# Optimization experiments

Hardware: AMD Instinct MI355X
Metric: run time of the kernel (lower is better)

Reference implementation:

```python
import jax, jax.numpy as jnp
import numpy as np

B, N, E = 2, 50000, 800000
IN, HID, OUT = 128, 64, 1
EPS = 1e-5


def setup_inputs() -> dict:
    key = jax.random.key(0)
    ks = jax.random.split(key, 13)
    x = jax.random.normal(ks[0], (B, N, IN), jnp.float32)
    edge_index = jax.random.randint(ks[1], (2, E), 0, N, dtype=jnp.int64)
    edge_weight = 0.1 * jax.random.normal(ks[2], (E,), jnp.float32)  # nn.Parameter, pre-exp
    W1 = jax.random.normal(ks[3], (IN, HID), jnp.float32) / np.sqrt(IN)
    b1 = jnp.zeros((HID,), jnp.float32)
    W2 = jax.random.normal(ks[4], (HID, HID), jnp.float32) / np.sqrt(HID)
    b2 = jnp.zeros((HID,), jnp.float32)
    g1 = jnp.ones((HID,), jnp.float32)
    be1 = jnp.zeros((HID,), jnp.float32)
    g2 = jnp.ones((HID,), jnp.float32)
    be2 = jnp.zeros((HID,), jnp.float32)
    Wc = jax.random.normal(ks[5], (HID, OUT), jnp.float32) / np.sqrt(HID)
    bc = jnp.zeros((OUT,), jnp.float32)
    return {"x": x, "edge_weight": edge_weight, "W1": W1, "b1": b1,
            "W2": W2, "b2": b2, "g1": g1, "be1": be1, "g2": g2, "be2": be2,
            "Wc": Wc, "bc": bc, "edge_index": edge_index}


def reference(x, edge_weight, W1, b1, W2, b2, g1, be1, g2, be2, Wc, bc, edge_index):
    n = x.shape[1]
    row, col = edge_index[0], edge_index[1]
    ew = jnp.exp(edge_weight)
    # GCN normalization with self-loops (fill_value=1), as in PyG gcn_norm
    loop = jnp.arange(n)
    rows = jnp.concatenate([row, loop])
    cols = jnp.concatenate([col, loop])
    w = jnp.concatenate([ew, jnp.ones((n,), ew.dtype)])
    deg = jax.ops.segment_sum(w, cols, num_segments=n)
    dinv = 1.0 / jnp.sqrt(deg)  # deg >= 1 due to self-loops
    norm = dinv[rows] * w * dinv[cols]  # [E+N]

    def conv(h, W, b):
        h = h @ W                                  # [B, N, H]
        msg = h[:, rows, :] * norm[None, :, None]  # gather + weight  [B, E+N, H]
        agg = jnp.zeros_like(h).at[:, cols, :].add(msg)  # scatter-add
        return agg + b

    def bn(h, g, be):  # BatchNorm1d over flattened (B*N, H), training-mode stats
        h2 = h.reshape(-1, h.shape[-1])
        m = h2.mean(axis=0)
        v = h2.var(axis=0)
        return (((h2 - m) / jnp.sqrt(v + EPS)) * g + be).reshape(h.shape)

    h = jax.nn.relu(conv(x, W1, b1))
    h = bn(h, g1, be1)  # dropout is identity in eval
    h = jax.nn.relu(conv(h, W2, b2))
    h = bn(h, g2, be2)
    out = (h @ Wc + bc)[..., 0]  # squeeze(-1) -> [B, N]
    return out
```

## Files before the change

### kernel.cpp

```cpp
#include <hip/hip_runtime.h>
#include <hip/hip_fp16.h>
#include <cstdint>
#include <cstddef>


#define CAP  64
#define OCAP 65536
#define BN_EPS 1e-5f

static __device__ __forceinline__ unsigned h2u(__half2 h) {
  union { __half2 h; unsigned u; } c; c.h = h; return c.u;
}
static __device__ __forceinline__ __half2 u2h(unsigned u) {
  union { unsigned u; __half2 h; } c; c.u = u; return c.h;
}
static __device__ __forceinline__ unsigned pack_pair(int src, float w) {
  __half hw = __float2half_rn(w);
  union { __half h; unsigned short s; } c; c.h = hw;
  return ((unsigned)src << 16) | c.s;
}
static __device__ __forceinline__ float pair_w(unsigned p) {
  union { unsigned short s; __half h; } c; c.s = (unsigned short)(p & 0xFFFFu);
  return __half2float(c.h);
}

__global__ void k_mega(const float* __restrict__ x, const float* __restrict__ W,
                       __half* __restrict__ out, int nrows, int N,
                       const float* __restrict__ ew, const int* __restrict__ ei,
                       int* __restrict__ cnt, unsigned* __restrict__ pairs,
                       int* __restrict__ ofl_cnt, int* __restrict__ ofl_list,
                       int E, int gemmBlocks, int fillBlocks) {
  constexpr int RT = 64, KC = 64, S = KC + 4;
  __shared__ float ws[KC * 64];
  __shared__ float xs[RT * S];

  int bid = blockIdx.x;
  int tid = threadIdx.x;
  int role = bid % 3;

  if (role == 0) {
    int gid = bid / 3;
    if (gid >= gemmBlocks) return;
    int row0 = gid * RT;
    int rg = tid >> 4, cg = tid & 15;
    int c0 = cg * 4, r0 = rg * 4;
    float acc[4][4];
#pragma unroll
    for (int i = 0; i < 4; ++i)
#pragma unroll
      for (int j = 0; j < 4; ++j) acc[i][j] = 0.0f;

    for (int ch = 0; ch < 2; ++ch) {
      if (ch) __syncthreads();
      const float4* Wp = (const float4*)(W + (size_t)ch * KC * 64);
      for (int s = tid; s < KC * 16; s += 256)
        ((float4*)ws)[s] = Wp[s];
      for (int s = tid; s < RT * 16; s += 256) {
        int r = s >> 4, k4 = s & 15;
        int gr = row0 + r;
        float4 v = make_float4(0.f, 0.f, 0.f, 0.f);
        if (gr < nrows)
          v = *(const float4*)(x + (size_t)gr * 128 + ch * KC + k4 * 4);
        *(float4*)&xs[r * S + k4 * 4] = v;
      }
      __syncthreads();
#pragma unroll 2
      for (int kk = 0; kk < KC; kk += 4) {
        float4 wv0 = *(const float4*)&ws[(kk + 0) * 64 + c0];
        float4 wv1 = *(const float4*)&ws[(kk + 1) * 64 + c0];
        float4 wv2 = *(const float4*)&ws[(kk + 2) * 64 + c0];
        float4 wv3 = *(const float4*)&ws[(kk + 3) * 64 + c0];
#pragma unroll
        for (int i = 0; i < 4; ++i) {
          float4 xv = *(const float4*)&xs[(r0 + i) * S + kk];
          acc[i][0] = fmaf(xv.x, wv0.x, acc[i][0]);
          acc[i][1] = fmaf(xv.x, wv0.y, acc[i][1]);
          acc[i][2] = fmaf(xv.x, wv0.z, acc[i][2]);
          acc[i][3] = fmaf(xv.x, wv0.w, acc[i][3]);
          acc[i][0] = fmaf(xv.y, wv1.x, acc[i][0]);
          acc[i][1] = fmaf(xv.y, wv1.y, acc[i][1]);
          acc[i][2] = fmaf(xv.y, wv1.z, acc[i][2]);
          acc[i][3] = fmaf(xv.y, wv1.w, acc[i][3]);
          acc[i][0] = fmaf(xv.z, wv2.x, acc[i][0]);
          acc[i][1] = fmaf(xv.z, wv2.y, acc[i][1]);
          acc[i][2] = fmaf(xv.z, wv2.z, acc[i][2]);
          acc[i][3] = fmaf(xv.z, wv2.w, acc[i][3]);
          acc[i][0] = fmaf(xv.w, wv3.x, acc[i][0]);
          acc[i][1] = fmaf(xv.w, wv3.y, acc[i][1]);
          acc[i][2] = fmaf(xv.w, wv3.z, acc[i][2]);
          acc[i][3] = fmaf(xv.w, wv3.w, acc[i][3]);
        }
      }
    }
#pragma unroll
    for (int i = 0; i < 4; ++i) {
      int gr = row0 + r0 + i;
      if (gr < nrows) {
        int orow = (gr < N) ? gr * 2 : (gr - N) * 2 + 1;
        __half2 h01 = __floats2half2_rn(acc[i][0], acc[i][1]);
        __half2 h23 = __floats2half2_rn(acc[i][2], acc[i][3]);
        *(uint2*)(out + (size_t)orow * 64 + c0) = make_uint2(h2u(h01), h2u(h23));
      }
    }
  } else {
    int fid = (bid / 3) * 2 + role - 1;
    if (fid >= fillBlocks) return;
    int e = fid * 256 + tid;
    if (e >= E) return;
    int r = ei[e];
    int c = ei[(size_t)E + e];
    float w = expf(ew[e]);
    int pos = atomicAdd(&cnt[c], 1);
    if (pos < CAP) {
      pairs[(size_t)c * CAP + pos] = pack_pair(r, w);
    } else {
      int o = atomicAdd(ofl_cnt, 1);
      if (o < OCAP) ofl_list[o] = e;
    }
  }
}

__global__ void k_degb(const unsigned* __restrict__ pairs, const int* __restrict__ cnt,
                       float* __restrict__ deg, int N) {
  int node = blockIdx.x * 4 + (threadIdx.x >> 6);
  if (node >= N) return;
  int lane = threadIdx.x & 63;
  int n = cnt[node];
  n = n > CAP ? CAP : n;
  float v = 0.0f;
  if (lane < n) v = pair_w(pairs[(size_t)node * CAP + lane]);
#pragma unroll
  for (int off = 32; off > 0; off >>= 1) v += __shfl_xor(v, off, 64);
  if (lane == 0) deg[node] = v + 1.0f;
}

__global__ void k_dego(const float* __restrict__ ew, const int* __restrict__ ei,
                       const int* __restrict__ ofl_cnt, const int* __restrict__ ofl_list,
                       float* __restrict__ deg, int E) {
  int tot = *ofl_cnt;
  if (tot > OCAP) tot = OCAP;
  for (int i = blockIdx.x * blockDim.x + threadIdx.x; i < tot;
       i += gridDim.x * blockDim.x) {
    int e = ofl_list[i];
    atomicAdd(&deg[ei[(size_t)E + e]], expf(ew[e]));
  }
}

__global__ void k_dinvf(float* __restrict__ deg, int N) {
  int i = blockIdx.x * blockDim.x + threadIdx.x;
  if (i < N) deg[i] = rsqrtf(deg[i]);
}

__global__ void k_gemm2(const __half* __restrict__ in, const float* __restrict__ W,
                        __half* __restrict__ out, int nrows,
                        const float* __restrict__ bias, const float* __restrict__ scsh) {
  constexpr int RT = 64, KC = 64, S = KC + 4;
  __shared__ float ws[KC * 64];
  __shared__ float xs[RT * S];

  int tid = threadIdx.x;
  int row0 = blockIdx.x * RT;
  for (int s = tid; s < KC * 16; s += 256)
    ((float4*)ws)[s] = ((const float4*)W)[s];
  for (int s = tid; s < RT * 16; s += 256) {
    int r = s >> 4, k4 = s & 15;
    int gr = row0 + r;
    int kg = k4 * 4;
    float4 v = make_float4(0.f, 0.f, 0.f, 0.f);
    if (gr < nrows) {
      uint2 u = *(const uint2*)(in + (size_t)gr * 64 + kg);
      float2 fa = __half22float2(u2h(u.x));
      float2 fb = __half22float2(u2h(u.y));
      v = make_float4(fa.x, fa.y, fb.x, fb.y);
    }
    float4 bb = *(const float4*)(bias + kg);
    float4 sc = *(const float4*)(scsh + kg);
    float4 sh = *(const float4*)(scsh + 64 + kg);
    v.x = fmaxf(v.x + bb.x, 0.f) * sc.x + sh.x;
    v.y = fmaxf(v.y + bb.y, 0.f) * sc.y + sh.y;
    v.z = fmaxf(v.z + bb.z, 0.f) * sc.z + sh.z;
    v.w = fmaxf(v.w + bb.w, 0.f) * sc.w + sh.w;
    *(float4*)&xs[r * S + kg] = v;
  }
  __syncthreads();

  int rg = tid >> 4, cg = tid & 15;
  int c0 = cg * 4, r0 = rg * 4;
  float acc[4][4];
#pragma unroll
  for (int i = 0; i < 4; ++i)
#pragma unroll
    for (int j = 0; j < 4; ++j) acc[i][j] = 0.0f;
#pragma unroll 2
  for (int kk = 0; kk < KC; kk += 4) {
    float4 wv0 = *(const float4*)&ws[(kk + 0) * 64 + c0];
    float4 wv1 = *(const float4*)&ws[(kk + 1) * 64 + c0];
    float4 wv2 = *(const float4*)&ws[(kk + 2) * 64 + c0];
    float4 wv3 = *(const float4*)&ws[(kk + 3) * 64 + c0];
#pragma unroll
    for (int i = 0; i < 4; ++i) {
      float4 xv = *(const float4*)&xs[(r0 + i) * S + kk];
      acc[i][0] = fmaf(xv.x, wv0.x, acc[i][0]);
      acc[i][1] = fmaf(xv.x, wv0.y, acc[i][1]);
      acc[i][2] = fmaf(xv.x, wv0.z, acc[i][2]);
      acc[i][3] = fmaf(xv.x, wv0.w, acc[i][3]);
      acc[i][0] = fmaf(xv.y, wv1.x, acc[i][0]);
      acc[i][1] = fmaf(xv.y, wv1.y, acc[i][1]);
      acc[i][2] = fmaf(xv.y, wv1.z, acc[i][2]);
      acc[i][3] = fmaf(xv.y, wv1.w, acc[i][3]);
      acc[i][0] = fmaf(xv.z, wv2.x, acc[i][0]);
      acc[i][1] = fmaf(xv.z, wv2.y, acc[i][1]);
      acc[i][2] = fmaf(xv.z, wv2.z, acc[i][2]);
      acc[i][3] = fmaf(xv.z, wv2.w, acc[i][3]);
      acc[i][0] = fmaf(xv.w, wv3.x, acc[i][0]);
      acc[i][1] = fmaf(xv.w, wv3.y, acc[i][1]);
      acc[i][2] = fmaf(xv.w, wv3.z, acc[i][2]);
      acc[i][3] = fmaf(xv.w, wv3.w, acc[i][3]);
    }
  }
#pragma unroll
  for (int i = 0; i < 4; ++i) {
    int gr = row0 + r0 + i;
    if (gr < nrows) {
      __half2 h01 = __floats2half2_rn(acc[i][0], acc[i][1]);
      __half2 h23 = __floats2half2_rn(acc[i][2], acc[i][3]);
      *(uint2*)(out + (size_t)gr * 64 + c0) = make_uint2(h2u(h01), h2u(h23));
    }
  }
}

__global__ void k_agg(const __half* __restrict__ h, const unsigned* __restrict__ pairs,
                      const int* __restrict__ cnt, const float* __restrict__ dinv,
                      __half* __restrict__ raw, int N) {
  int node = blockIdx.x * 4 + (threadIdx.x >> 6);
  if (node >= N) return;
  int lane = threadIdx.x & 63;
  const __half2* hv = (const __half2*)h;
  float dc = dinv[node];
  float2 self = __half22float2(hv[(size_t)node * 64 + lane]);
  float2 acc = make_float2(self.x * dc, self.y * dc);
  int n = cnt[node];
  n = n > CAP ? CAP : n;
  const unsigned* pp = pairs + (size_t)node * CAP;
  int k = 0;
  for (; k + 12 <= n; k += 12) {
    unsigned p[12];
#pragma unroll
    for (int q = 0; q < 12; ++q) p[q] = pp[k + q];
    float dr[12];
#pragma unroll
    for (int q = 0; q < 12; ++q) dr[q] = dinv[p[q] >> 16];
    __half2 v[12];
#pragma unroll
    for (int q = 0; q < 12; ++q) v[q] = hv[(size_t)(p[q] >> 16) * 64 + lane];
#pragma unroll
    for (int q = 0; q < 12; ++q) {
      float w = pair_w(p[q]) * dr[q];
      float2 f = __half22float2(v[q]);
      acc.x = fmaf(w, f.x, acc.x);
      acc.y = fmaf(w, f.y, acc.y);
    }
  }
  for (; k + 4 <= n; k += 4) {
    unsigned p[4];
#pragma unroll
    for (int q = 0; q < 4; ++q) p[q] = pp[k + q];
    float dr[4];
#pragma unroll
    for (int q = 0; q < 4; ++q) dr[q] = dinv[p[q] >> 16];
    __half2 v[4];
#pragma unroll
    for (int q = 0; q < 4; ++q) v[q] = hv[(size_t)(p[q] >> 16) * 64 + lane];
#pragma unroll
    for (int q = 0; q < 4; ++q) {
      float w = pair_w(p[q]) * dr[q];
      float2 f = __half22float2(v[q]);
      acc.x = fmaf(w, f.x, acc.x);
      acc.y = fmaf(w, f.y, acc.y);
    }
  }
  for (; k < n; ++k) {
    unsigned p = pp[k];
    float w = pair_w(p) * dinv[p >> 16];
    float2 f = __half22float2(hv[(size_t)(p >> 16) * 64 + lane]);
    acc.x = fmaf(w, f.x, acc.x);
    acc.y = fmaf(w, f.y, acc.y);
  }
  ((__half2*)raw)[(size_t)node * 64 + lane] =
      __floats2half2_rn(acc.x * dc, acc.y * dc);
}

__global__ void k_ofl(const float* __restrict__ ew, const int* __restrict__ ei,
                      const float* __restrict__ dinv, const int* __restrict__ ofl_cnt,
                      const int* __restrict__ ofl_list,
                      const __half* __restrict__ h, __half* __restrict__ raw,
                      int N, int E) {
  int tot = *ofl_cnt;
  if (tot > OCAP) tot = OCAP;
  for (int i = blockIdx.x * blockDim.x + threadIdx.x; i < tot;
       i += gridDim.x * blockDim.x) {
    int e = ofl_list[i];
    int r = ei[e];
    int c = ei[(size_t)E + e];
    float nrm = dinv[r] * expf(ew[e]) * dinv[c];
    const __half2* hr = (const __half2*)(h + (size_t)r * 128);
    unsigned* dst = (unsigned*)(raw + (size_t)c * 128);
    for (int j = 0; j < 64; ++j) {
      float2 hv2 = __half22float2(hr[j]);
      unsigned old = dst[j], assumed;
      do {
        assumed = old;
        float2 cur = __half22float2(u2h(assumed));
        __half2 nv = __floats2half2_rn(cur.x + nrm * hv2.x, cur.y + nrm * hv2.y);
        old = atomicCAS(&dst[j], assumed, h2u(nv));
      } while (old != assumed);
    }
  }
}

__global__ void k_stats(const __half* __restrict__ raw, const float* __restrict__ bias,
                        float* __restrict__ stats, const float* __restrict__ g,
                        const float* __restrict__ be, float* __restrict__ scsh,
                        int* __restrict__ done, float invCnt, int rows) {
  __shared__ float S[256], Q[256];
  __shared__ int isLast;
  int tid = threadIdx.x;
  int c = tid & 63, rg = tid >> 6;
  float s = 0.0f, q = 0.0f;
  for (int r = blockIdx.x * 4 + rg; r < rows; r += gridDim.x * 4) {
    float y = fmaxf(__half2float(raw[(size_t)r * 64 + c]) + bias[c], 0.0f);
    s += y;
    q += y * y;
  }
  S[tid] = s; Q[tid] = q;
  __syncthreads();
  if (tid < 64) {
    float ts = S[tid] + S[tid + 64] + S[tid + 128] + S[tid + 192];
    float tq = Q[tid] + Q[tid + 64] + Q[tid + 128] + Q[tid + 192];
    atomicAdd(&stats[tid], ts);
    atomicAdd(&stats[64 + tid], tq);
  }
  __threadfence();
  if (tid == 0) {
    int old = atomicAdd(done, 1);
    isLast = (old == (int)gridDim.x - 1);
  }
  __syncthreads();
  if (isLast && tid < 64) {
    __threadfence();
    float m = atomicAdd(&stats[tid], 0.0f) * invCnt;
    float qq = atomicAdd(&stats[64 + tid], 0.0f) * invCnt;
    float v = qq - m * m;
    v = v < 0.0f ? 0.0f : v;
    float inv = rsqrtf(v + BN_EPS);
    float sc = g[tid] * inv;
    scsh[tid] = sc;
    scsh[64 + tid] = be[tid] - m * sc;
  }
}

__global__ void k_out(const __half* __restrict__ raw, const float* __restrict__ bias,
                      const float* __restrict__ scsh, const float* __restrict__ Wc,
                      const float* __restrict__ bc, float* __restrict__ out,
                      int rows, int N) {
  int row = blockIdx.x * 4 + (threadIdx.x >> 6);
  int c = threadIdx.x & 63;
  if (row >= rows) return;
  float v = fmaxf(__half2float(raw[(size_t)row * 64 + c]) + bias[c], 0.0f)
              * scsh[c] + scsh[64 + c];
  float p = v * Wc[c];
#pragma unroll
  for (int off = 32; off > 0; off >>= 1) p += __shfl_xor(p, off, 64);
  if (c == 0) {
    int node = row >> 1, b = row & 1;
    out[(size_t)b * N + node] = p + bc[0];
  }
}

extern "C" void kernel_launch(void* const* d_in, const int* in_sizes, int n_in,
                              void* d_out, int out_size, void* d_ws, size_t ws_size,
                              hipStream_t stream) {
  const float* x   = (const float*)d_in[0];
  const float* ew  = (const float*)d_in[1];
  const float* W1  = (const float*)d_in[2];
  const float* b1  = (const float*)d_in[3];
  const float* W2  = (const float*)d_in[4];
  const float* b2  = (const float*)d_in[5];
  const float* g1  = (const float*)d_in[6];
  const float* be1 = (const float*)d_in[7];
  const float* g2  = (const float*)d_in[8];
  const float* be2 = (const float*)d_in[9];
  const float* Wc  = (const float*)d_in[10];
  const float* bc  = (const float*)d_in[11];
  const int*   ei  = (const int*)d_in[12];

  const int E  = in_sizes[1];
  const int BN = in_sizes[0] / 128;
  const int N  = BN / 2;

  char* w = (char*)d_ws;
  size_t off = 0;
  int*   cnt    = (int*)  (w + off); off += (size_t)N * 4;
  float* stats1 = (float*)(w + off); off += 512;
  float* stats2 = (float*)(w + off); off += 512;
  int*   oflc   = (int*)  (w + off); off += 16;
  int*   done1  = (int*)  (w + off); off += 16;
  int*   done2  = (int*)  (w + off); off += 16;
  size_t zbytes = off;
  float* dinv   = (float*)(w + off); off += (size_t)N * 4;
  float* scsh1  = (float*)(w + off); off += 512;
  float* scsh2  = (float*)(w + off); off += 512;
  int*   ofll   = (int*)  (w + off); off += (size_t)OCAP * 4;
  off = (off + 255) & ~(size_t)255;
  unsigned* pairs = (unsigned*)(w + off); off += (size_t)N * CAP * 4;
  __half* bufA  = (__half*)(w + off); off += (size_t)BN * 64 * 2;
  __half* bufB  = (__half*)(w + off); off += (size_t)BN * 64 * 2;

  float* out = (float*)d_out;

  hipMemsetAsync(w, 0, zbytes, stream);

  dim3 blk(256);
  int gB = (BN + 63) / 64;
  int fB = (E + 255) / 256;
  int base3 = gB > (fB + 1) / 2 ? gB : (fB + 1) / 2;
  int gMega = 3 * base3;
  int gN  = (N + 255) / 256;
  int gR  = (BN + 3) / 4;
  int gA  = (N + 3) / 4;

  k_mega<<<gMega, blk, 0, stream>>>(x, W1, bufA, BN, N, ew, ei, cnt, pairs,
                                    oflc, ofll, E, gB, fB);
  k_degb<<<gA, blk, 0, stream>>>(pairs, cnt, dinv, N);
  k_dego<<<16, blk, 0, stream>>>(ew, ei, oflc, ofll, dinv, E);
  k_dinvf<<<gN, blk, 0, stream>>>(dinv, N);

  k_agg<<<gA, blk, 0, stream>>>(bufA, pairs, cnt, dinv, bufB, N);
  k_ofl<<<16, blk, 0, stream>>>(ew, ei, dinv, oflc, ofll, bufA, bufB, N, E);
  k_stats<<<400, blk, 0, stream>>>(bufB, b1, stats1, g1, be1, scsh1, done1,
                                   1.0f / (float)BN, BN);

  k_gemm2<<<gB, blk, 0, stream>>>(bufB, W2, bufA, BN, b1, scsh1);
  k_agg<<<gA, blk, 0, stream>>>(bufA, pairs, cnt, dinv, bufB, N);
  k_ofl<<<16, blk, 0, stream>>>(ew, ei, dinv, oflc, ofll, bufA, bufB, N, E);
  k_stats<<<400, blk, 0, stream>>>(bufB, b2, stats2, g2, be2, scsh2, done2,
                                   1.0f / (float)BN, BN);

  k_out<<<gR, blk, 0, stream>>>(bufB, b2, scsh2, Wc, bc, out, BN, N);
}
```

Measured before the change: 366.5 us.

## Fuse BN statistics into aggregation, add overflow fast-paths, persistent two-node agg waves

Folds the BatchNorm statistics pass into the aggregation kernel, so each wave accumulates per-channel sum and sum-of-squares while writing results, and the last block computes scale and shift. This removes a separate full read of the activation buffer. The overflow path returns early when no edge overflowed, and in that case the rsqrt is done inside the degree kernel instead of a separate pass. The aggregation becomes a persistent grid of 1024 blocks where each wave handles two nodes at once, giving more independent gathers in flight but predicated loads when the two nodes have different degrees. If overflow edges exist, a single last block recomputes the statistics serially over all rows, which would be slow.

```diff
diff --git a/kernel.cpp b/kernel.cpp
--- a/kernel.cpp
+++ b/kernel.cpp
@@ -121,7 +121,7 @@
 }
 
 __global__ void k_degb(const unsigned* __restrict__ pairs, const int* __restrict__ cnt,
-                       float* __restrict__ deg, int N) {
+                       const int* __restrict__ ofl_cnt, float* __restrict__ deg, int N) {
   int node = blockIdx.x * 4 + (threadIdx.x >> 6);
   if (node >= N) return;
   int lane = threadIdx.x & 63;
@@ -131,13 +131,14 @@
   if (lane < n) v = pair_w(pairs[(size_t)node * CAP + lane]);
 #pragma unroll
   for (int off = 32; off > 0; off >>= 1) v += __shfl_xor(v, off, 64);
-  if (lane == 0) deg[node] = v + 1.0f;
+  if (lane == 0) deg[node] = (*ofl_cnt == 0) ? rsqrtf(v + 1.0f) : (v + 1.0f);
 }
 
 __global__ void k_dego(const float* __restrict__ ew, const int* __restrict__ ei,
                        const int* __restrict__ ofl_cnt, const int* __restrict__ ofl_list,
                        float* __restrict__ deg, int E) {
   int tot = *ofl_cnt;
+  if (tot == 0) return;
   if (tot > OCAP) tot = OCAP;
   for (int i = blockIdx.x * blockDim.x + threadIdx.x; i < tot;
        i += gridDim.x * blockDim.x) {
@@ -146,9 +147,173 @@
   }
 }
 
-__global__ void k_dinvf(float* __restrict__ deg, int N) {
+__global__ void k_dinvf(float* __restrict__ deg, const int* __restrict__ ofl_cnt, int N) {
+  if (*ofl_cnt == 0) return;
   int i = blockIdx.x * blockDim.x + threadIdx.x;
   if (i < N) deg[i] = rsqrtf(deg[i]);
+}
+
+__global__ void k_agg(const __half* __restrict__ h, const unsigned* __restrict__ pairs,
+                      const int* __restrict__ cnt, const float* __restrict__ dinv,
+                      __half* __restrict__ raw, const float* __restrict__ bias,
+                      float* __restrict__ stats, const float* __restrict__ g,
+                      const float* __restrict__ be, float* __restrict__ scsh,
+                      int* __restrict__ done, float invCnt, int N) {
+  __shared__ float Ss[64][8], Qq[64][8];
+  __shared__ int isLast;
+  const int tid = threadIdx.x, lane = tid & 63;
+  const int nwav = gridDim.x * 4;
+  const int gw = blockIdx.x * 4 + (tid >> 6);
+  const __half2* hv = (const __half2*)h;
+  __half2* rv = (__half2*)raw;
+  int l5 = lane & 31;
+  int ch0 = 2 * l5;
+  float bb0 = bias[ch0], bb1 = bias[ch0 + 1];
+  float sx = 0.f, sy = 0.f, qx = 0.f, qy = 0.f;
+
+  for (int t = gw; 2 * t < N; t += nwav) {
+    int node0 = 2 * t, node1 = 2 * t + 1;
+    bool has1 = node1 < N;
+    float dc0 = dinv[node0];
+    float dc1 = has1 ? dinv[node1] : 0.f;
+    float2 s0 = __half22float2(hv[(size_t)node0 * 64 + lane]);
+    float2 s1 = has1 ? __half22float2(hv[(size_t)node1 * 64 + lane])
+                     : make_float2(0.f, 0.f);
+    float a0x = s0.x * dc0, a0y = s0.y * dc0;
+    float a1x = s1.x * dc1, a1y = s1.y * dc1;
+    int n0 = cnt[node0]; n0 = n0 > CAP ? CAP : n0;
+    int n1 = has1 ? cnt[node1] : 0; n1 = n1 > CAP ? CAP : n1;
+    const unsigned* pp0 = pairs + (size_t)node0 * CAP;
+    const unsigned* pp1 = pairs + (size_t)node1 * CAP;
+    int nmax = n0 > n1 ? n0 : n1;
+    for (int k = 0; k < nmax; k += 8) {
+      unsigned pr0[8], pr1[8];
+#pragma unroll
+      for (int q = 0; q < 8; ++q) {
+        pr0[q] = pp0[(k + q < n0) ? k + q : 0];
+        pr1[q] = pp1[(k + q < n1) ? k + q : 0];
+      }
+      float w0[8], w1[8];
+#pragma unroll
+      for (int q = 0; q < 8; ++q) {
+        w0[q] = (k + q < n0) ? pair_w(pr0[q]) * dinv[pr0[q] >> 16] : 0.f;
+        w1[q] = (k + q < n1) ? pair_w(pr1[q]) * dinv[pr1[q] >> 16] : 0.f;
+      }
+      __half2 v0[8], v1[8];
+#pragma unroll
+      for (int q = 0; q < 8; ++q) {
+        v0[q] = hv[(size_t)(pr0[q] >> 16) * 64 + lane];
+        v1[q] = hv[(size_t)(pr1[q] >> 16) * 64 + lane];
+      }
+#pragma unroll
+      for (int q = 0; q < 8; ++q) {
+        float2 f0 = __half22float2(v0[q]);
+        float2 f1 = __half22float2(v1[q]);
+        a0x = fmaf(w0[q], f0.x, a0x); a0y = fmaf(w0[q], f0.y, a0y);
+        a1x = fmaf(w1[q], f1.x, a1x); a1y = fmaf(w1[q], f1.y, a1y);
+      }
+    }
+    __half2 r0 = __floats2half2_rn(a0x * dc0, a0y * dc0);
+    rv[(size_t)node0 * 64 + lane] = r0;
+    float2 f0 = __half22float2(r0);
+    float y0 = fmaxf(f0.x + bb0, 0.f), y1 = fmaxf(f0.y + bb1, 0.f);
+    sx += y0; qx += y0 * y0; sy += y1; qy += y1 * y1;
+    if (has1) {
+      __half2 r1 = __floats2half2_rn(a1x * dc1, a1y * dc1);
+      rv[(size_t)node1 * 64 + lane] = r1;
+      float2 f1 = __half22float2(r1);
+      float z0 = fmaxf(f1.x + bb0, 0.f), z1 = fmaxf(f1.y + bb1, 0.f);
+      sx += z0; qx += z0 * z0; sy += z1; qy += z1 * z1;
+    }
+  }
+
+  int j = tid >> 5;
+  Ss[ch0][j] = sx; Ss[ch0 + 1][j] = sy;
+  Qq[ch0][j] = qx; Qq[ch0 + 1][j] = qy;
+  __syncthreads();
+  if (tid < 64) {
+    float s = 0.f, q = 0.f;
+#pragma unroll
+    for (int u = 0; u < 8; ++u) { s += Ss[tid][u]; q += Qq[tid][u]; }
+    atomicAdd(&stats[tid], s);
+    atomicAdd(&stats[64 + tid], q);
+  }
+  __threadfence();
+  if (tid == 0) {
+    int old = atomicAdd(done, 1);
+    isLast = (old == (int)gridDim.x - 1);
+  }
+  __syncthreads();
+  if (isLast && tid < 64) {
+    __threadfence();
+    float m = atomicAdd(&stats[tid], 0.0f) * invCnt;
+    float qq = atomicAdd(&stats[64 + tid], 0.0f) * invCnt;
+    float v = qq - m * m;
+    v = v < 0.f ? 0.f : v;
+    float inv = rsqrtf(v + BN_EPS);
+    float sc = g[tid] * inv;
+    scsh[tid] = sc;
+    scsh[64 + tid] = be[tid] - m * sc;
+  }
+}
+
+__global__ void k_ofl(const float* __restrict__ ew, const int* __restrict__ ei,
+                      const float* __restrict__ dinv, const int* __restrict__ ofl_cnt,
+                      const int* __restrict__ ofl_list,
+                      const __half* __restrict__ h, __half* __restrict__ raw,
+                      const float* __restrict__ bias, const float* __restrict__ g,
+                      const float* __restrict__ be, float* __restrict__ scsh,
+                      int* __restrict__ done, float invCnt, int rows, int E) {
+  int tot = *ofl_cnt;
+  if (tot == 0) return;
+  if (tot > OCAP) tot = OCAP;
+  __shared__ float S[256], Q[256];
+  __shared__ int isLast;
+  int tid = threadIdx.x;
+  for (int i = blockIdx.x * 256 + tid; i < tot; i += gridDim.x * 256) {
+    int e = ofl_list[i];
+    int r = ei[e], c = ei[(size_t)E + e];
+    float nrm = dinv[r] * expf(ew[e]) * dinv[c];
+    const __half2* hr = (const __half2*)(h + (size_t)r * 128);
+    unsigned* dst = (unsigned*)(raw + (size_t)c * 128);
+    for (int jj = 0; jj < 64; ++jj) {
+      float2 hv2 = __half22float2(hr[jj]);
+      unsigned old = dst[jj], assumed;
+      do {
+        assumed = old;
+        float2 cur = __half22float2(u2h(assumed));
+        __half2 nv = __floats2half2_rn(cur.x + nrm * hv2.x, cur.y + nrm * hv2.y);
+        old = atomicCAS(&dst[jj], assumed, h2u(nv));
+      } while (old != assumed);
+    }
+  }
+  __threadfence();
+  if (tid == 0) {
+    int old = atomicAdd(done, 1);
+    isLast = (old == (int)gridDim.x - 1);
+  }
+  __syncthreads();
+  if (!isLast) return;
+  __threadfence();
+  int c = tid & 63, rg = tid >> 6;
+  float s = 0.f, q = 0.f;
+  for (int r = rg; r < rows; r += 4) {
+    float y = fmaxf(__half2float(raw[(size_t)r * 64 + c]) + bias[c], 0.f);
+    s += y; q += y * y;
+  }
+  S[tid] = s; Q[tid] = q;
+  __syncthreads();
+  if (tid < 64) {
+    float ts = S[tid] + S[tid + 64] + S[tid + 128] + S[tid + 192];
+    float tq = Q[tid] + Q[tid + 64] + Q[tid + 128] + Q[tid + 192];
+    float m = ts * invCnt;
+    float v = tq * invCnt - m * m;
+    v = v < 0.f ? 0.f : v;
+    float inv = rsqrtf(v + BN_EPS);
+    float sc = g[tid] * inv;
+    scsh[tid] = sc;
+    scsh[64 + tid] = be[tid] - m * sc;
+  }
 }
 
 __global__ void k_gemm2(const __half* __restrict__ in, const float* __restrict__ W,
@@ -229,136 +394,6 @@
   }
 }
 
-__global__ void k_agg(const __half* __restrict__ h, const unsigned* __restrict__ pairs,
-                      const int* __restrict__ cnt, const float* __restrict__ dinv,
-                      __half* __restrict__ raw, int N) {
-  int node = blockIdx.x * 4 + (threadIdx.x >> 6);
-  if (node >= N) return;
-  int lane = threadIdx.x & 63;
-  const __half2* hv = (const __half2*)h;
-  float dc = dinv[node];
-  float2 self = __half22float2(hv[(size_t)node * 64 + lane]);
-  float2 acc = make_float2(self.x * dc, self.y * dc);
-  int n = cnt[node];
-  n = n > CAP ? CAP : n;
-  const unsigned* pp = pairs + (size_t)node * CAP;
-  int k = 0;
-  for (; k + 12 <= n; k += 12) {
-    unsigned p[12];
-#pragma unroll
-    for (int q = 0; q < 12; ++q) p[q] = pp[k + q];
-    float dr[12];
-#pragma unroll
-    for (int q = 0; q < 12; ++q) dr[q] = dinv[p[q] >> 16];
-    __half2 v[12];
-#pragma unroll
-    for (int q = 0; q < 12; ++q) v[q] = hv[(size_t)(p[q] >> 16) * 64 + lane];
-#pragma unroll
-    for (int q = 0; q < 12; ++q) {
-      float w = pair_w(p[q]) * dr[q];
-      float2 f = __half22float2(v[q]);
-      acc.x = fmaf(w, f.x, acc.x);
-      acc.y = fmaf(w, f.y, acc.y);
-    }
-  }
-  for (; k + 4 <= n; k += 4) {
-    unsigned p[4];
-#pragma unroll
-    for (int q = 0; q < 4; ++q) p[q] = pp[k + q];
-    float dr[4];
-#pragma unroll
-    for (int q = 0; q < 4; ++q) dr[q] = dinv[p[q] >> 16];
-    __half2 v[4];
-#pragma unroll
-    for (int q = 0; q < 4; ++q) v[q] = hv[(size_t)(p[q] >> 16) * 64 + lane];
-#pragma unroll
-    for (int q = 0; q < 4; ++q) {
-      float w = pair_w(p[q]) * dr[q];
-      float2 f = __half22float2(v[q]);
-      acc.x = fmaf(w, f.x, acc.x);
-      acc.y = fmaf(w, f.y, acc.y);
-    }
-  }
-  for (; k < n; ++k) {
-    unsigned p = pp[k];
-    float w = pair_w(p) * dinv[p >> 16];
-    float2 f = __half22float2(hv[(size_t)(p >> 16) * 64 + lane]);
-    acc.x = fmaf(w, f.x, acc.x);
-    acc.y = fmaf(w, f.y, acc.y);
-  }
-  ((__half2*)raw)[(size_t)node * 64 + lane] =
-      __floats2half2_rn(acc.x * dc, acc.y * dc);
-}
-
-__global__ void k_ofl(const float* __restrict__ ew, const int* __restrict__ ei,
-                      const float* __restrict__ dinv, const int* __restrict__ ofl_cnt,
-                      const int* __restrict__ ofl_list,
-                      const __half* __restrict__ h, __half* __restrict__ raw,
-                      int N, int E) {
-  int tot = *ofl_cnt;
-  if (tot > OCAP) tot = OCAP;
-  for (int i = blockIdx.x * blockDim.x + threadIdx.x; i < tot;
-       i += gridDim.x * blockDim.x) {
-    int e = ofl_list[i];
-    int r = ei[e];
-    int c = ei[(size_t)E + e];
-    float nrm = dinv[r] * expf(ew[e]) * dinv[c];
-    const __half2* hr = (const __half2*)(h + (size_t)r * 128);
-    unsigned* dst = (unsigned*)(raw + (size_t)c * 128);
-    for (int j = 0; j < 64; ++j) {
-      float2 hv2 = __half22float2(hr[j]);
-      unsigned old = dst[j], assumed;
-      do {
-        assumed = old;
-        float2 cur = __half22float2(u2h(assumed));
-        __half2 nv = __floats2half2_rn(cur.x + nrm * hv2.x, cur.y + nrm * hv2.y);
-        old = atomicCAS(&dst[j], assumed, h2u(nv));
-      } while (old != assumed);
-    }
-  }
-}
-
-__global__ void k_stats(const __half* __restrict__ raw, const float* __restrict__ bias,
-                        float* __restrict__ stats, const float* __restrict__ g,
-                        const float* __restrict__ be, float* __restrict__ scsh,
-                        int* __restrict__ done, float invCnt, int rows) {
-  __shared__ float S[256], Q[256];
-  __shared__ int isLast;
-  int tid = threadIdx.x;
-  int c = tid & 63, rg = tid >> 6;
-  float s = 0.0f, q = 0.0f;
-  for (int r = blockIdx.x * 4 + rg; r < rows; r += gridDim.x * 4) {
-    float y = fmaxf(__half2float(raw[(size_t)r * 64 + c]) + bias[c], 0.0f);
-    s += y;
-    q += y * y;
-  }
-  S[tid] = s; Q[tid] = q;
-  __syncthreads();
-  if (tid < 64) {
-    float ts = S[tid] + S[tid + 64] + S[tid + 128] + S[tid + 192];
-    float tq = Q[tid] + Q[tid + 64] + Q[tid + 128] + Q[tid + 192];
-    atomicAdd(&stats[tid], ts);
-    atomicAdd(&stats[64 + tid], tq);
-  }
-  __threadfence();
-  if (tid == 0) {
-    int old = atomicAdd(done, 1);
-    isLast = (old == (int)gridDim.x - 1);
-  }
-  __syncthreads();
-  if (isLast && tid < 64) {
-    __threadfence();
-    float m = atomicAdd(&stats[tid], 0.0f) * invCnt;
-    float qq = atomicAdd(&stats[64 + tid], 0.0f) * invCnt;
-    float v = qq - m * m;
-    v = v < 0.0f ? 0.0f : v;
-    float inv = rsqrtf(v + BN_EPS);
-    float sc = g[tid] * inv;
-    scsh[tid] = sc;
-    scsh[64 + tid] = be[tid] - m * sc;
-  }
-}
-
 __global__ void k_out(const __half* __restrict__ raw, const float* __restrict__ bias,
                       const float* __restrict__ scsh, const float* __restrict__ Wc,
                       const float* __restrict__ bc, float* __restrict__ out,
@@ -406,6 +441,8 @@
   int*   oflc   = (int*)  (w + off); off += 16;
   int*   done1  = (int*)  (w + off); off += 16;
   int*   done2  = (int*)  (w + off); off += 16;
+  int*   odone1 = (int*)  (w + off); off += 16;
+  int*   odone2 = (int*)  (w + off); off += 16;
   size_t zbytes = off;
   float* dinv   = (float*)(w + off); off += (size_t)N * 4;
   float* scsh1  = (float*)(w + off); off += 512;
@@ -427,24 +464,26 @@
   int gMega = 3 * base3;
   int gN  = (N + 255) / 256;
   int gR  = (BN + 3) / 4;
-  int gA  = (N + 3) / 4;
+  int gD  = (N + 3) / 4;
+  int gAgg = 1024;
+  float invCnt = 1.0f / (float)BN;
 
   k_mega<<<gMega, blk, 0, stream>>>(x, W1, bufA, BN, N, ew, ei, cnt, pairs,
                                     oflc, ofll, E, gB, fB);
-  k_degb<<<gA, blk, 0, stream>>>(pairs, cnt, dinv, N);
+  k_degb<<<gD, blk, 0, stream>>>(pairs, cnt, oflc, dinv, N);
   k_dego<<<16, blk, 0, stream>>>(ew, ei, oflc, ofll, dinv, E);
-  k_dinvf<<<gN, blk, 0, stream>>>(dinv, N);
-
-  k_agg<<<gA, blk, 0, stream>>>(bufA, pairs, cnt, dinv, bufB, N);
-  k_ofl<<<16, blk, 0, stream>>>(ew, ei, dinv, oflc, ofll, bufA, bufB, N, E);
-  k_stats<<<400, blk, 0, stream>>>(bufB, b1, stats1, g1, be1, scsh1, done1,
-                                   1.0f / (float)BN, BN);
+  k_dinvf<<<gN, blk, 0, stream>>>(dinv, oflc, N);
+
+  k_agg<<<gAgg, blk, 0, stream>>>(bufA, pairs, cnt, dinv, bufB, b1,
+                                  stats1, g1, be1, scsh1, done1, invCnt, N);
+  k_ofl<<<64, blk, 0, stream>>>(ew, ei, dinv, oflc, ofll, bufA, bufB,
+                                b1, g1, be1, scsh1, odone1, invCnt, BN, E);
 
   k_gemm2<<<gB, blk, 0, stream>>>(bufB, W2, bufA, BN, b1, scsh1);
-  k_agg<<<gA, blk, 0, stream>>>(bufA, pairs, cnt, dinv, bufB, N);
-  k_ofl<<<16, blk, 0, stream>>>(ew, ei, dinv, oflc, ofll, bufA, bufB, N, E);
-  k_stats<<<400, blk, 0, stream>>>(bufB, b2, stats2, g2, be2, scsh2, done2,
-                                   1.0f / (float)BN, BN);
+  k_agg<<<gAgg, blk, 0, stream>>>(bufA, pairs, cnt, dinv, bufB, b2,
+                                  stats2, g2, be2, scsh2, done2, invCnt, N);
+  k_ofl<<<64, blk, 0, stream>>>(ew, ei, dinv, oflc, ofll, bufA, bufB,
+                                b2, g2, be2, scsh2, odone2, invCnt, BN, E);
 
   k_out<<<gR, blk, 0, stream>>>(bufB, b2, scsh2, Wc, bc, out, BN, N);
 }
```

Result: slower. 519.6 us (+41.8%).

## Fuse BN stats into aggregation and fold degree/overflow kernels into fewer launches

Applied to the files above, without the earlier changes.

Computes per-block BatchNorm partial sums inside the aggregation kernel, so the separate pass that re-reads the aggregated buffer is gone; a small 64-block kernel reduces those partials into scale/shift. The degree, overflow-degree and rsqrt kernels are merged into one, with a last-block path used only when overflow edges exist; overflow aggregation and a full stats recompute are likewise moved into a last-block fallback. This removes several launches and one full read of the activations per layer, but the overflow path now runs serially in a single block.

```diff
diff --git a/kernel.cpp b/kernel.cpp
--- a/kernel.cpp
+++ b/kernel.cpp
@@ -121,34 +121,198 @@
 }
 
 __global__ void k_degb(const unsigned* __restrict__ pairs, const int* __restrict__ cnt,
-                       float* __restrict__ deg, int N) {
-  int node = blockIdx.x * 4 + (threadIdx.x >> 6);
-  if (node >= N) return;
-  int lane = threadIdx.x & 63;
-  int n = cnt[node];
-  n = n > CAP ? CAP : n;
-  float v = 0.0f;
-  if (lane < n) v = pair_w(pairs[(size_t)node * CAP + lane]);
-#pragma unroll
-  for (int off = 32; off > 0; off >>= 1) v += __shfl_xor(v, off, 64);
-  if (lane == 0) deg[node] = v + 1.0f;
-}
-
-__global__ void k_dego(const float* __restrict__ ew, const int* __restrict__ ei,
-                       const int* __restrict__ ofl_cnt, const int* __restrict__ ofl_list,
-                       float* __restrict__ deg, int E) {
+                       const int* __restrict__ ofl_cnt, float* __restrict__ deg,
+                       int* __restrict__ done, int N,
+                       const float* __restrict__ ew, const int* __restrict__ ei,
+                       const int* __restrict__ ofl_list, int E) {
+  int tid = threadIdx.x;
+  int node = blockIdx.x * 4 + (tid >> 6);
+  int lane = tid & 63;
   int tot = *ofl_cnt;
+  if (node < N) {
+    int n = cnt[node];
+    n = n > CAP ? CAP : n;
+    float v = 0.0f;
+    if (lane < n) v = pair_w(pairs[(size_t)node * CAP + lane]);
+#pragma unroll
+    for (int off = 32; off > 0; off >>= 1) v += __shfl_xor(v, off, 64);
+    if (lane == 0) deg[node] = (tot == 0) ? rsqrtf(v + 1.0f) : (v + 1.0f);
+  }
+  if (tot == 0) return;
   if (tot > OCAP) tot = OCAP;
-  for (int i = blockIdx.x * blockDim.x + threadIdx.x; i < tot;
-       i += gridDim.x * blockDim.x) {
+  __shared__ int isLast;
+  __threadfence();
+  if (tid == 0) isLast = (atomicAdd(done, 1) == (int)gridDim.x - 1);
+  __syncthreads();
+  if (!isLast) return;
+  for (int i = tid; i < tot; i += 256) {
     int e = ofl_list[i];
     atomicAdd(&deg[ei[(size_t)E + e]], expf(ew[e]));
   }
-}
-
-__global__ void k_dinvf(float* __restrict__ deg, int N) {
-  int i = blockIdx.x * blockDim.x + threadIdx.x;
-  if (i < N) deg[i] = rsqrtf(deg[i]);
+  __threadfence();
+  __syncthreads();
+  for (int i = tid; i < N; i += 256) deg[i] = rsqrtf(deg[i]);
+}
+
+__global__ void k_agg(const __half* __restrict__ h, const unsigned* __restrict__ pairs,
+                      const int* __restrict__ cnt, const float* __restrict__ dinv,
+                      __half* __restrict__ raw, const float* __restrict__ bias,
+                      float* __restrict__ pst, int N) {
+  __shared__ float Ss[64][9], Qq[64][9];
+  const int tid = threadIdx.x, lane = tid & 63;
+  int node = blockIdx.x * 4 + (tid >> 6);
+  const __half2* hv = (const __half2*)h;
+  int ch0 = 2 * (lane & 31);
+  float sx = 0.f, sy = 0.f, qx = 0.f, qy = 0.f;
+
+  if (node < N) {
+    float dc = dinv[node];
+    float2 self = __half22float2(hv[(size_t)node * 64 + lane]);
+    float ax = self.x * dc, ay = self.y * dc;
+    int n = cnt[node];
+    n = n > CAP ? CAP : n;
+    const unsigned* pp = pairs + (size_t)node * CAP;
+    int k = 0;
+    for (; k + 12 <= n; k += 12) {
+      unsigned pr[12];
+#pragma unroll
+      for (int q = 0; q < 12; ++q) pr[q] = pp[k + q];
+      float dr[12];
+#pragma unroll
+      for (int q = 0; q < 12; ++q) dr[q] = dinv[pr[q] >> 16];
+      __half2 v[12];
+#pragma unroll
+      for (int q = 0; q < 12; ++q) v[q] = hv[(size_t)(pr[q] >> 16) * 64 + lane];
+#pragma unroll
+      for (int q = 0; q < 12; ++q) {
+        float w = pair_w(pr[q]) * dr[q];
+        float2 f = __half22float2(v[q]);
+        ax = fmaf(w, f.x, ax);
+        ay = fmaf(w, f.y, ay);
+      }
+    }
+    for (; k + 4 <= n; k += 4) {
+      unsigned pr[4];
+#pragma unroll
+      for (int q = 0; q < 4; ++q) pr[q] = pp[k + q];
+      float dr[4];
+#pragma unroll
+      for (int q = 0; q < 4; ++q) dr[q] = dinv[pr[q] >> 16];
+      __half2 v[4];
+#pragma unroll
+      for (int q = 0; q < 4; ++q) v[q] = hv[(size_t)(pr[q] >> 16) * 64 + lane];
+#pragma unroll
+      for (int q = 0; q < 4; ++q) {
+        float w = pair_w(pr[q]) * dr[q];
+        float2 f = __half22float2(v[q]);
+        ax = fmaf(w, f.x, ax);
+        ay = fmaf(w, f.y, ay);
+      }
+    }
+    for (; k < n; ++k) {
+      unsigned pr = pp[k];
+      float w = pair_w(pr) * dinv[pr >> 16];
+      float2 f = __half22float2(hv[(size_t)(pr >> 16) * 64 + lane]);
+      ax = fmaf(w, f.x, ax);
+      ay = fmaf(w, f.y, ay);
+    }
+    __half2 r = __floats2half2_rn(ax * dc, ay * dc);
+    ((__half2*)raw)[(size_t)node * 64 + lane] = r;
+    float2 f = __half22float2(r);
+    float bb0 = bias[ch0], bb1 = bias[ch0 + 1];
+    float y0 = fmaxf(f.x + bb0, 0.f), y1 = fmaxf(f.y + bb1, 0.f);
+    sx = y0; qx = y0 * y0; sy = y1; qy = y1 * y1;
+  }
+
+  int j = tid >> 5;
+  Ss[ch0][j] = sx; Ss[ch0 + 1][j] = sy;
+  Qq[ch0][j] = qx; Qq[ch0 + 1][j] = qy;
+  __syncthreads();
+  if (tid < 64) {
+    float s = 0.f, q = 0.f;
+#pragma unroll
+    for (int u = 0; u < 8; ++u) { s += Ss[tid][u]; q += Qq[tid][u]; }
+    pst[(size_t)blockIdx.x * 128 + tid] = s;
+    pst[(size_t)blockIdx.x * 128 + 64 + tid] = q;
+  }
+}
+
+__global__ void k_scsh(const float* __restrict__ pst, int nblk,
+                       const float* __restrict__ g, const float* __restrict__ be,
+                       float* __restrict__ scsh, int* __restrict__ done, float invCnt,
+                       const float* __restrict__ ew, const int* __restrict__ ei,
+                       const float* __restrict__ dinv, const int* __restrict__ ofl_cnt,
+                       const int* __restrict__ ofl_list,
+                       const __half* __restrict__ h, __half* __restrict__ raw,
+                       const float* __restrict__ bias, int rows, int E) {
+  __shared__ float S[256], Q[256];
+  __shared__ int isLast;
+  int tid = threadIdx.x, ch = blockIdx.x;
+  float s = 0.f, q = 0.f;
+  for (int b = tid; b < nblk; b += 256) {
+    s += pst[(size_t)b * 128 + ch];
+    q += pst[(size_t)b * 128 + 64 + ch];
+  }
+  S[tid] = s; Q[tid] = q;
+  __syncthreads();
+  for (int o = 128; o; o >>= 1) {
+    if (tid < o) { S[tid] += S[tid + o]; Q[tid] += Q[tid + o]; }
+    __syncthreads();
+  }
+  if (tid == 0) {
+    float m = S[0] * invCnt;
+    float v = Q[0] * invCnt - m * m;
+    v = v < 0.f ? 0.f : v;
+    float inv = rsqrtf(v + BN_EPS);
+    float sc = g[ch] * inv;
+    scsh[ch] = sc;
+    scsh[64 + ch] = be[ch] - m * sc;
+  }
+  int tot = *ofl_cnt;
+  if (tot == 0) return;
+  if (tot > OCAP) tot = OCAP;
+  __threadfence();
+  if (tid == 0) isLast = (atomicAdd(done, 1) == (int)gridDim.x - 1);
+  __syncthreads();
+  if (!isLast) return;
+  for (int i = tid; i < tot; i += 256) {
+    int e = ofl_list[i];
+    int r = ei[e], c = ei[(size_t)E + e];
+    float nrm = dinv[r] * expf(ew[e]) * dinv[c];
+    const __half2* hr = (const __half2*)(h + (size_t)r * 128);
+    unsigned* dst = (unsigned*)(raw + (size_t)c * 128);
+    for (int jj = 0; jj < 64; ++jj) {
+      float2 hv2 = __half22float2(hr[jj]);
+      unsigned old = dst[jj], assumed;
+      do {
+        assumed = old;
+        float2 cur = __half22float2(u2h(assumed));
+        __half2 nv = __floats2half2_rn(cur.x + nrm * hv2.x, cur.y + nrm * hv2.y);
+        old = atomicCAS(&dst[jj], assumed, h2u(nv));
+      } while (old != assumed);
+    }
+  }
+  __threadfence();
+  __syncthreads();
+  int c = tid & 63, rg = tid >> 6;
+  float s2 = 0.f, q2 = 0.f;
+  for (int r = rg; r < rows; r += 4) {
+    float y = fmaxf(__half2float(raw[(size_t)r * 64 + c]) + bias[c], 0.f);
+    s2 += y; q2 += y * y;
+  }
+  S[tid] = s2; Q[tid] = q2;
+  __syncthreads();
+  if (tid < 64) {
+    float ts = S[tid] + S[tid + 64] + S[tid + 128] + S[tid + 192];
+    float tq = Q[tid] + Q[tid + 64] + Q[tid + 128] + Q[tid + 192];
+    float m = ts * invCnt;
+    float v = tq * invCnt - m * m;
+    v = v < 0.f ? 0.f : v;
+    float inv = rsqrtf(v + BN_EPS);
+    float sc = g[tid] * inv;
+    scsh[tid] = sc;
+    scsh[64 + tid] = be[tid] - m * sc;
+  }
 }
 
 __global__ void k_gemm2(const __half* __restrict__ in, const float* __restrict__ W,
@@ -229,136 +393,6 @@
   }
 }
 
-__global__ void k_agg(const __half* __restrict__ h, const unsigned* __restrict__ pairs,
-                      const int* __restrict__ cnt, const float* __restrict__ dinv,
-                      __half* __restrict__ raw, int N) {
-  int node = blockIdx.x * 4 + (threadIdx.x >> 6);
-  if (node >= N) return;
-  int lane = threadIdx.x & 63;
-  const __half2* hv = (const __half2*)h;
-  float dc = dinv[node];
-  float2 self = __half22float2(hv[(size_t)node * 64 + lane]);
-  float2 acc = make_float2(self.x * dc, self.y * dc);
-  int n = cnt[node];
-  n = n > CAP ? CAP : n;
-  const unsigned* pp = pairs + (size_t)node * CAP;
-  int k = 0;
-  for (; k + 12 <= n; k += 12) {
-    unsigned p[12];
-#pragma unroll
-    for (int q = 0; q < 12; ++q) p[q] = pp[k + q];
-    float dr[12];
-#pragma unroll
-    for (int q = 0; q < 12; ++q) dr[q] = dinv[p[q] >> 16];
-    __half2 v[12];
-#pragma unroll
-    for (int q = 0; q < 12; ++q) v[q] = hv[(size_t)(p[q] >> 16) * 64 + lane];
-#pragma unroll
-    for (int q = 0; q < 12; ++q) {
-      float w = pair_w(p[q]) * dr[q];
-      float2 f = __half22float2(v[q]);
-      acc.x = fmaf(w, f.x, acc.x);
-      acc.y = fmaf(w, f.y, acc.y);
-    }
-  }
-  for (; k + 4 <= n; k += 4) {
-    unsigned p[4];
-#pragma unroll
-    for (int q = 0; q < 4; ++q) p[q] = pp[k + q];
-    float dr[4];
-#pragma unroll
-    for (int q = 0; q < 4; ++q) dr[q] = dinv[p[q] >> 16];
-    __half2 v[4];
-#pragma unroll
-    for (int q = 0; q < 4; ++q) v[q] = hv[(size_t)(p[q] >> 16) * 64 + lane];
-#pragma unroll
-    for (int q = 0; q < 4; ++q) {
-      float w = pair_w(p[q]) * dr[q];
-      float2 f = __half22float2(v[q]);
-      acc.x = fmaf(w, f.x, acc.x);
-      acc.y = fmaf(w, f.y, acc.y);
-    }
-  }
-  for (; k < n; ++k) {
-    unsigned p = pp[k];
-    float w = pair_w(p) * dinv[p >> 16];
-    float2 f = __half22float2(hv[(size_t)(p >> 16) * 64 + lane]);
-    acc.x = fmaf(w, f.x, acc.x);
-    acc.y = fmaf(w, f.y, acc.y);
-  }
-  ((__half2*)raw)[(size_t)node * 64 + lane] =
-      __floats2half2_rn(acc.x * dc, acc.y * dc);
-}
-
-__global__ void k_ofl(const float* __restrict__ ew, const int* __restrict__ ei,
-                      const float* __restrict__ dinv, const int* __restrict__ ofl_cnt,
-                      const int* __restrict__ ofl_list,
-                      const __half* __restrict__ h, __half* __restrict__ raw,
-                      int N, int E) {
-  int tot = *ofl_cnt;
-  if (tot > OCAP) tot = OCAP;
-  for (int i = blockIdx.x * blockDim.x + threadIdx.x; i < tot;
-       i += gridDim.x * blockDim.x) {
-    int e = ofl_list[i];
-    int r = ei[e];
-    int c = ei[(size_t)E + e];
-    float nrm = dinv[r] * expf(ew[e]) * dinv[c];
-    const __half2* hr = (const __half2*)(h + (size_t)r * 128);
-    unsigned* dst = (unsigned*)(raw + (size_t)c * 128);
-    for (int j = 0; j < 64; ++j) {
-      float2 hv2 = __half22float2(hr[j]);
-      unsigned old = dst[j], assumed;
-      do {
-        assumed = old;
-        float2 cur = __half22float2(u2h(assumed));
-        __half2 nv = __floats2half2_rn(cur.x + nrm * hv2.x, cur.y + nrm * hv2.y);
-        old = atomicCAS(&dst[j], assumed, h2u(nv));
-      } while (old != assumed);
-    }
-  }
-}
-
-__global__ void k_stats(const __half* __restrict__ raw, const float* __restrict__ bias,
-                        float* __restrict__ stats, const float* __restrict__ g,
-                        const float* __restrict__ be, float* __restrict__ scsh,
-                        int* __restrict__ done, float invCnt, int rows) {
-  __shared__ float S[256], Q[256];
-  __shared__ int isLast;
-  int tid = threadIdx.x;
-  int c = tid & 63, rg = tid >> 6;
-  float s = 0.0f, q = 0.0f;
-  for (int r = blockIdx.x * 4 + rg; r < rows; r += gridDim.x * 4) {
-    float y = fmaxf(__half2float(raw[(size_t)r * 64 + c]) + bias[c], 0.0f);
-    s += y;
-    q += y * y;
-  }
-  S[tid] = s; Q[tid] = q;
-  __syncthreads();
-  if (tid < 64) {
-    float ts = S[tid] + S[tid + 64] + S[tid + 128] + S[tid + 192];
-    float tq = Q[tid] + Q[tid + 64] + Q[tid + 128] + Q[tid + 192];
-    atomicAdd(&stats[tid], ts);
-    atomicAdd(&stats[64 + tid], tq);
-  }
-  __threadfence();
-  if (tid == 0) {
-    int old = atomicAdd(done, 1);
-    isLast = (old == (int)gridDim.x - 1);
-  }
-  __syncthreads();
-  if (isLast && tid < 64) {
-    __threadfence();
-    float m = atomicAdd(&stats[tid], 0.0f) * invCnt;
-    float qq = atomicAdd(&stats[64 + tid], 0.0f) * invCnt;
-    float v = qq - m * m;
-    v = v < 0.0f ? 0.0f : v;
-    float inv = rsqrtf(v + BN_EPS);
-    float sc = g[tid] * inv;
-    scsh[tid] = sc;
-    scsh[64 + tid] = be[tid] - m * sc;
-  }
-}
-
 __global__ void k_out(const __half* __restrict__ raw, const float* __restrict__ bias,
                       const float* __restrict__ scsh, const float* __restrict__ Wc,
                       const float* __restrict__ bc, float* __restrict__ out,
@@ -401,17 +435,18 @@
   char* w = (char*)d_ws;
   size_t off = 0;
   int*   cnt    = (int*)  (w + off); off += (size_t)N * 4;
-  float* stats1 = (float*)(w + off); off += 512;
-  float* stats2 = (float*)(w + off); off += 512;
   int*   oflc   = (int*)  (w + off); off += 16;
-  int*   done1  = (int*)  (w + off); off += 16;
-  int*   done2  = (int*)  (w + off); off += 16;
+  int*   dbdone = (int*)  (w + off); off += 16;
+  int*   sdone1 = (int*)  (w + off); off += 16;
+  int*   sdone2 = (int*)  (w + off); off += 16;
   size_t zbytes = off;
   float* dinv   = (float*)(w + off); off += (size_t)N * 4;
   float* scsh1  = (float*)(w + off); off += 512;
   float* scsh2  = (float*)(w + off); off += 512;
   int*   ofll   = (int*)  (w + off); off += (size_t)OCAP * 4;
   off = (off + 255) & ~(size_t)255;
+  int gA = (N + 3) / 4;
+  float* pst    = (float*)(w + off); off += (size_t)gA * 128 * 4;
   unsigned* pairs = (unsigned*)(w + off); off += (size_t)N * CAP * 4;
   __half* bufA  = (__half*)(w + off); off += (size_t)BN * 64 * 2;
   __half* bufB  = (__half*)(w + off); off += (size_t)BN * 64 * 2;
@@ -425,26 +460,21 @@
   int fB = (E + 255) / 256;
   int base3 = gB > (fB + 1) / 2 ? gB : (fB + 1) / 2;
   int gMega = 3 * base3;
-  int gN  = (N + 255) / 256;
   int gR  = (BN + 3) / 4;
-  int gA  = (N + 3) / 4;
+  float invCnt = 1.0f / (float)BN;
 
   k_mega<<<gMega, blk, 0, stream>>>(x, W1, bufA, BN, N, ew, ei, cnt, pairs,
                                     oflc, ofll, E, gB, fB);
-  k_degb<<<gA, blk, 0, stream>>>(pairs, cnt, dinv, N);
-  k_dego<<<16, blk, 0, stream>>>(ew, ei, oflc, ofll, dinv, E);
-  k_dinvf<<<gN, blk, 0, stream>>>(dinv, N);
-
-  k_agg<<<gA, blk, 0, stream>>>(bufA, pairs, cnt, dinv, bufB, N);
-  k_ofl<<<16, blk, 0, stream>>>(ew, ei, dinv, oflc, ofll, bufA, bufB, N, E);
-  k_stats<<<400, blk, 0, stream>>>(bufB, b1, stats1, g1, be1, scsh1, done1,
-                                   1.0f / (float)BN, BN);
+  k_degb<<<gA, blk, 0, stream>>>(pairs, cnt, oflc, dinv, dbdone, N, ew, ei, ofll, E);
+
+  k_agg<<<gA, blk, 0, stream>>>(bufA, pairs, cnt, dinv, bufB, b1, pst, N);
+  k_scsh<<<64, blk, 0, stream>>>(pst, gA, g1, be1, scsh1, sdone1, invCnt,
+                                 ew, ei, dinv, oflc, ofll, bufA, bufB, b1, BN, E);
 
   k_gemm2<<<gB, blk, 0, stream>>>(bufB, W2, bufA, BN, b1, scsh1);
-  k_agg<<<gA, blk, 0, stream>>>(bufA, pairs, cnt, dinv, bufB, N);
-  k_ofl<<<16, blk, 0, stream>>>(ew, ei, dinv, oflc, ofll, bufA, bufB, N, E);
-  k_stats<<<400, blk, 0, stream>>>(bufB, b2, stats2, g2, be2, scsh2, done2,
-                                   1.0f / (float)BN, BN);
+  k_agg<<<gA, blk, 0, stream>>>(bufA, pairs, cnt, dinv, bufB, b2, pst, N);
+  k_scsh<<<64, blk, 0, stream>>>(pst, gA, g2, be2, scsh2, sdone2, invCnt,
+                                 ew, ei, dinv, oflc, ofll, bufA, bufB, b2, BN, E);
 
   k_out<<<gR, blk, 0, stream>>>(bufB, b2, scsh2, Wc, bc, out, BN, N);
 }
```

Result: faster. 348.5 us, median of 2 (-4.9%).
